# Performance work log

Hardware: AMD Instinct MI355X
Metric: run time of the kernel (lower is better)

## Reference

```python
import jax, jax.numpy as jnp
import numpy as np

N_NODES = 50000
N_EDGES = 800000
IN_F = 64
OUT_F = 64
N_REL = 32
N_BASES = 30


def setup_inputs() -> dict:
    key = jax.random.key(0)
    ks = jax.random.split(key, 6)
    x = jax.random.normal(ks[0], (N_NODES, IN_F), dtype=jnp.float32)
    edge_index = jax.random.randint(ks[1], (2, N_EDGES), 0, N_NODES, dtype=jnp.int64)
    edge_type = jax.random.randint(ks[2], (N_EDGES,), 0, N_REL, dtype=jnp.int64)
    basis = jax.random.normal(ks[3], (N_BASES, IN_F, OUT_F), dtype=jnp.float32) * 0.01
    coeff = jax.random.normal(ks[4], (N_REL, N_BASES), dtype=jnp.float32) * 0.01
    self_weight = jax.random.normal(ks[5], (IN_F, OUT_F), dtype=jnp.float32) * 0.01
    bias = jnp.zeros((OUT_F,), dtype=jnp.float32)
    return {"x": x, "edge_index": edge_index, "edge_type": edge_type,
            "num_nodes": N_NODES, "basis": basis, "coeff": coeff,
            "self_weight": self_weight, "bias": bias}


def reference(x, edge_index, edge_type, num_nodes, basis, coeff, self_weight, bias):
    # W_r = sum_b coeff[r,b] * basis[b]  -> (R, in, out)
    rel_weight = jnp.einsum('rb,bio->rio', coeff, basis)
    source_idx = edge_index[0]
    target_idx = edge_index[1]
    src_feats = x[source_idx]  # (E, in)

    def body(out, rw_r):
        rw, r = rw_r
        mask = (edge_type == r).astype(jnp.float32)  # (E,)
        msg = (src_feats @ rw) * mask[:, None]       # (E, out)
        return out.at[target_idx].add(msg), None

    out0 = jnp.zeros((num_nodes, rel_weight.shape[-1]), dtype=jnp.float32)
    out, _ = jax.lax.scan(body, out0, (rel_weight, jnp.arange(rel_weight.shape[0])))

    in_degree = jnp.zeros((num_nodes,), dtype=jnp.float32).at[target_idx].add(1.0)
    in_degree = jnp.maximum(in_degree, 1.0)
    out = out / in_degree[:, None]
    out = out + x @ self_weight + bias
    return out
```

## Files before the change

### kernel.cpp

```cpp
#include <hip/hip_runtime.h>
#include <hip/hip_bf16.h>

#define IN_F   64
#define OUT_F  64
#define N_RELS 32
#define N_BAS  30
#define KROW   2048
#define B1CHUNK 4096

typedef __attribute__((ext_vector_type(8))) short short8v;
typedef __attribute__((ext_vector_type(4))) _Float16 half4v;
typedef __attribute__((ext_vector_type(4))) float f32x4;
typedef __attribute__((ext_vector_type(4))) unsigned u32x4;
typedef __attribute__((ext_vector_type(2))) unsigned u32x2;

#define MFMA16(a, b, c) __builtin_amdgcn_mfma_f32_16x16x16f16(a, b, c, 0, 0, 0)

__device__ __forceinline__ int dmin(int a, int b) { return a < b ? a : b; }
__device__ __forceinline__ unsigned short f2bf(float f) {
    __hip_bfloat16 h = __float2bfloat16(f);
    return *(unsigned short*)&h;
}

__global__ void __launch_bounds__(256)
k_prep(const float* __restrict__ basis, const float* __restrict__ sw,
       const float* __restrict__ bias, __hip_bfloat16* __restrict__ bbT,
       const float* __restrict__ x, unsigned* __restrict__ xh,
       const int* __restrict__ tgt, int* __restrict__ gsum,
       int N, int E, int nxp) {
    int bb = blockIdx.x;
    int tid = threadIdx.x;
    if (bb < 512) {
        int idx = bb * 256 + tid;
        int e = idx & 7, lane = (idx >> 3) & 63, s = (idx >> 9) & 15, kq = (idx >> 13) & 3, cb = idx >> 15;
        int l15 = lane & 15, lk = lane >> 4;
        int o = cb * 16 + l15;
        int k = kq * 512 + s * 32 + lk * 8 + e;
        int b = k >> 6, i = k & 63;
        float v;
        if (b < N_BAS)      v = basis[((size_t)b * IN_F + i) * OUT_F + o];
        else if (b == 30)   v = sw[(size_t)i * OUT_F + o];
        else                v = (i == 0) ? bias[o] : 0.f;
        bbT[idx] = __float2bfloat16(v);
    } else if (bb < 512 + nxp) {
        int idx = (bb - 512) * 256 + tid;
        if (idx < (N + 1) * 32) {
            int g = idx & 31, n = idx >> 5;
            unsigned v = 0;
            if (n < N) {
                int f = (g & 15) + ((g >> 4) << 5);
                _Float16 lo = (_Float16)x[((size_t)n << 6) + f];
                _Float16 hi = (_Float16)x[((size_t)n << 6) + f + 16];
                v = (unsigned)*(unsigned short*)&lo | ((unsigned)*(unsigned short*)&hi << 16);
            }
            xh[idx] = v;
        }
    } else {
        __shared__ int lh[256];
        int vb = bb - 512 - nxp;
        lh[tid] = 0;
        __syncthreads();
        for (int i = vb * 256 + tid; i < E; i += 256 * 256)
            atomicAdd(&lh[tgt[i] >> 8], 1);
        __syncthreads();
        if (lh[tid]) atomicAdd(&gsum[tid], lh[tid]);
    }
}

__global__ void k_scanB(const int* __restrict__ gsum, int* __restrict__ gexcl,
                        int* __restrict__ bcur, int* __restrict__ off, int NB, int N) {
    int l = threadIdx.x;
    int a0 = (4*l+0 < NB) ? gsum[4*l+0] : 0;
    int a1 = (4*l+1 < NB) ? gsum[4*l+1] : 0;
    int a2 = (4*l+2 < NB) ? gsum[4*l+2] : 0;
    int a3 = (4*l+3 < NB) ? gsum[4*l+3] : 0;
    int s = a0 + a1 + a2 + a3;
    int sc = s;
    for (int d = 1; d < 64; d <<= 1) {
        int o = __shfl_up(sc, d, 64);
        if (l >= d) sc += o;
    }
    int base = sc - s;
    if (4*l+0 < NB) { gexcl[4*l+0] = base;          bcur[4*l+0] = base; }
    if (4*l+1 < NB) { gexcl[4*l+1] = base+a0;       bcur[4*l+1] = base+a0; }
    if (4*l+2 < NB) { gexcl[4*l+2] = base+a0+a1;    bcur[4*l+2] = base+a0+a1; }
    if (4*l+3 < NB) { gexcl[4*l+3] = base+a0+a1+a2; bcur[4*l+3] = base+a0+a1+a2; }
    if (l == 63) { gexcl[NB] = sc; off[N] = sc; }
}

__global__ void __launch_bounds__(1024)
k_b1(const int* __restrict__ src, const int* __restrict__ tgt, const int* __restrict__ et,
     int* __restrict__ bcur, unsigned* __restrict__ ssr, int E) {
    __shared__ unsigned ls_p[B1CHUNK];
    __shared__ unsigned char ls_b[B1CHUNK];
    __shared__ int lh[256], lbase[256], gbase[256], lcur[256];
    int tid = threadIdx.x;
    int e0 = blockIdx.x * B1CHUNK;
    int n = E - e0; if (n > B1CHUNK) n = B1CHUNK;
    if (tid < 256) { lh[tid] = 0; lcur[tid] = 0; }
    __syncthreads();
    unsigned pr[4]; int br[4];
#pragma unroll
    for (int k = 0; k < 4; ++k) {
        int i = k * 1024 + tid;
        br[k] = -1;
        if (i < n) {
            int t = tgt[e0 + i];
            br[k] = t >> 8;
            pr[k] = ((unsigned)(t & 255) << 21) | ((unsigned)src[e0 + i] << 5) | (unsigned)et[e0 + i];
            atomicAdd(&lh[br[k]], 1);
        }
    }
    __syncthreads();
    if (tid < 64) {
        int a0 = lh[4*tid], a1 = lh[4*tid+1], a2 = lh[4*tid+2], a3 = lh[4*tid+3];
        int s = a0 + a1 + a2 + a3, sc = s;
        for (int d = 1; d < 64; d <<= 1) {
            int o = __shfl_up(sc, d, 64);
            if (tid >= d) sc += o;
        }
        int base = sc - s;
        lbase[4*tid] = base; lbase[4*tid+1] = base+a0;
        lbase[4*tid+2] = base+a0+a1; lbase[4*tid+3] = base+a0+a1+a2;
    }
    __syncthreads();
    if (tid < 256 && lh[tid]) gbase[tid] = atomicAdd(&bcur[tid], lh[tid]);
    __syncthreads();
#pragma unroll
    for (int k = 0; k < 4; ++k) {
        if (br[k] >= 0) {
            int pos = atomicAdd(&lcur[br[k]], 1);
            int s = lbase[br[k]] + pos;
            ls_p[s] = pr[k];
            ls_b[s] = (unsigned char)br[k];
        }
    }
    __syncthreads();
#pragma unroll
    for (int k = 0; k < 4; ++k) {
        int i = k * 1024 + tid;
        if (i < n) {
            int b = ls_b[i];
            ssr[gbase[b] + (i - lbase[b])] = ls_p[i];
        }
    }
}

__global__ void __launch_bounds__(256)
k_b2(const unsigned* __restrict__ ssr, const int* __restrict__ gexcl,
     int* __restrict__ off, unsigned* __restrict__ ssr2, int N) {
    __shared__ int lh[256], lofs[256], lcur[256];
    int g = blockIdx.x, tid = threadIdx.x;
    int o0 = gexcl[g], o1 = gexcl[g + 1];
    lh[tid] = 0;
    __syncthreads();
    for (int i = o0 + tid; i < o1; i += 256)
        atomicAdd(&lh[ssr[i] >> 21], 1);
    __syncthreads();
    if (tid < 64) {
        int a0 = lh[4*tid], a1 = lh[4*tid+1], a2 = lh[4*tid+2], a3 = lh[4*tid+3];
        int s = a0 + a1 + a2 + a3, sc = s;
        for (int d = 1; d < 64; d <<= 1) {
            int o = __shfl_up(sc, d, 64);
            if (tid >= d) sc += o;
        }
        int base = sc - s;
        lofs[4*tid] = base; lofs[4*tid+1] = base+a0;
        lofs[4*tid+2] = base+a0+a1; lofs[4*tid+3] = base+a0+a1+a2;
    }
    __syncthreads();
    int t = (g << 8) + tid;
    if (t < N) off[t] = o0 + lofs[tid];
    lcur[tid] = o0 + lofs[tid];
    __syncthreads();
    for (int i = o0 + tid; i < o1; i += 256) {
        unsigned p = ssr[i];
        int pos = atomicAdd(&lcur[p >> 21], 1);
        ssr2[pos] = p;
    }
}

__device__ __forceinline__ void edge_round(
    unsigned char* zb, const unsigned* cofs2, const unsigned* est,
    const unsigned* __restrict__ ssr2, const char* __restrict__ xhB,
    int tIdx, int s0r, int s1r, float xselfv,
    int mh, int l15, int lk, unsigned xadd2, unsigned cbase, u32x4 w0)
{
    int deg = s1r - s0r;
    int sbase = lk << 2;
    f32x4 acc00 = {0.f,0.f,0.f,0.f};
    f32x4 acc01 = acc00, acc10 = acc00, acc11 = acc00;
    if (deg > 0) {
        if (deg <= 128) {
            int nt = (deg + 15) >> 4;
#pragma unroll 1
            for (int kt = 0; kt < nt; ++kt) {
                u32x4 wn = w0;
                if (kt + 1 < nt)
                    wn = *(const u32x4*)((const unsigned char*)(est + tIdx * 128 + (kt + 1) * 16 + sbase));
                union { unsigned short u[4]; half4v h; } bf0, bf1, a0, a1;
#pragma unroll
                for (int j = 0; j < 4; ++j) {
                    unsigned wj = w0[j];
                    unsigned bw = cofs2[cbase + ((wj & 31u) << 4) + l15];
                    unsigned xw = *(const unsigned*)(xhB + (((size_t)((wj >> 5) & 0xFFFFu)) << 7) + xadd2);
                    bf0.u[j] = (unsigned short)(bw & 0xFFFFu);
                    bf1.u[j] = (unsigned short)(bw >> 16);
                    a0.u[j]  = (unsigned short)(xw & 0xFFFFu);
                    a1.u[j]  = (unsigned short)(xw >> 16);
                }
                acc00 = MFMA16(a0.h, bf0.h, acc00);
                acc01 = MFMA16(a0.h, bf1.h, acc01);
                acc10 = MFMA16(a1.h, bf0.h, acc10);
                acc11 = MFMA16(a1.h, bf1.h, acc11);
                w0 = wn;
            }
        } else {
            int last = s1r - 1;
#pragma unroll 1
            for (int kt = 0; kt * 16 < deg; ++kt) {
                int rem = deg - kt * 16;
                unsigned ew = ssr2[dmin(s0r + kt * 16 + l15, last)];
                union { unsigned short u[4]; half4v h; } bf0, bf1, a0, a1;
#pragma unroll
                for (int j = 0; j < 4; ++j) {
                    unsigned wj = (unsigned)__builtin_amdgcn_ds_bpermute((lk << 4) + j * 4, (int)ew);
                    bool okj = (sbase + j) < rem;
                    unsigned rrow = okj ? (wj & 31u) : 32u;
                    unsigned wjs  = okj ? wj : 0u;
                    unsigned bw = cofs2[cbase + (rrow << 4) + l15];
                    unsigned xw = *(const unsigned*)(xhB + (((size_t)((wjs >> 5) & 0xFFFFu)) << 7) + xadd2);
                    bf0.u[j] = (unsigned short)(bw & 0xFFFFu);
                    bf1.u[j] = (unsigned short)(bw >> 16);
                    a0.u[j]  = (unsigned short)(xw & 0xFFFFu);
                    a1.u[j]  = (unsigned short)(xw >> 16);
                }
                acc00 = MFMA16(a0.h, bf0.h, acc00);
                acc01 = MFMA16(a0.h, bf1.h, acc01);
                acc10 = MFMA16(a1.h, bf0.h, acc10);
                acc11 = MFMA16(a1.h, bf1.h, acc11);
            }
        }
    }
    float inv = 1.f / fmaxf((float)deg, 1.f);
    unsigned rb = (unsigned)tIdx << 12;
    unsigned swz = (unsigned)((tIdx & 7) << 4);
    unsigned ib = (unsigned)((mh << 5) + (lk << 2));
    {
        unsigned short h0, h1, h2, h3;
        u32x2 pv;
        h0 = f2bf(acc00[0]*inv); h1 = f2bf(acc00[1]*inv); h2 = f2bf(acc00[2]*inv); h3 = f2bf(acc00[3]*inv);
        pv[0] = h0 | ((unsigned)h1 << 16); pv[1] = h2 | ((unsigned)h3 << 16);
        unsigned byt = ((unsigned)l15 << 7) + (ib << 1);
        byt ^= swz ^ (((byt >> 7) & 7) << 4);
        *(u32x2*)(zb + rb + byt) = pv;
        h0 = f2bf(acc01[0]*inv); h1 = f2bf(acc01[1]*inv); h2 = f2bf(acc01[2]*inv); h3 = f2bf(acc01[3]*inv);
        pv[0] = h0 | ((unsigned)h1 << 16); pv[1] = h2 | ((unsigned)h3 << 16);
        byt = ((unsigned)(16 + l15) << 7) + (ib << 1);
        byt ^= swz ^ (((byt >> 7) & 7) << 4);
        *(u32x2*)(zb + rb + byt) = pv;
        h0 = f2bf(acc10[0]*inv); h1 = f2bf(acc10[1]*inv); h2 = f2bf(acc10[2]*inv); h3 = f2bf(acc10[3]*inv);
        pv[0] = h0 | ((unsigned)h1 << 16); pv[1] = h2 | ((unsigned)h3 << 16);
        byt = ((unsigned)l15 << 7) + ((ib + 16) << 1);
        byt ^= swz ^ (((byt >> 7) & 7) << 4);
        *(u32x2*)(zb + rb + byt) = pv;
        h0 = f2bf(acc11[0]*inv); h1 = f2bf(acc11[1]*inv); h2 = f2bf(acc11[2]*inv); h3 = f2bf(acc11[3]*inv);
        pv[0] = h0 | ((unsigned)h1 << 16); pv[1] = h2 | ((unsigned)h3 << 16);
        byt = ((unsigned)(16 + l15) << 7) + ((ib + 16) << 1);
        byt ^= swz ^ (((byt >> 7) & 7) << 4);
        *(u32x2*)(zb + rb + byt) = pv;
    }
    int lane = (lk << 4) + l15;
    if (lane < 32) {
        unsigned byt = (30u << 7) + ((unsigned)((mh << 5) + lane) << 1);
        byt ^= swz ^ (((byt >> 7) & 7) << 4);
        *(unsigned short*)(zb + rb + byt) = f2bf(xselfv);
        if (mh == 0 && lane == 0) {
            unsigned byb = (31u << 7);
            byb ^= swz ^ (((byb >> 7) & 7) << 4);
            *(unsigned short*)(zb + rb + byb) = (unsigned short)0x3F80;
        }
    }
}

__global__ void __launch_bounds__(1024, 8)
k_fused(const float* __restrict__ x, const unsigned* __restrict__ xh,
        const unsigned* __restrict__ ssr2, const int* __restrict__ off,
        const float* __restrict__ coeff, const __hip_bfloat16* __restrict__ bbT,
        float* __restrict__ out, int N) {
    __shared__ __align__(16) unsigned char zb[16 * 4096];
    __shared__ __align__(16) float pf[16 * 256];
    unsigned* cofs2 = (unsigned*)pf;
    unsigned* est   = ((unsigned*)pf) + 1120;
    int tid = threadIdx.x;
    int w = tid >> 6, lane = tid & 63;
    int mh = w & 1;
    int t0 = blockIdx.x * 16;

    int tA = t0 + (w >> 1), tB = tA + 8;
    int okA = (tA < N), okB = (tB < N);
    int offA0 = okA ? off[tA] : 0;
    int offA1 = okA ? off[tA + 1] : 0;
    int offB0 = okB ? off[tB] : 0;
    int offB1 = okB ? off[tB + 1] : 0;
    float xsA = okA ? x[((size_t)tA << 6) + (mh << 5) + (lane & 31)] : 0.f;
    float xsB = okB ? x[((size_t)tB << 6) + (mh << 5) + (lane & 31)] : 0.f;

    int s0A = __builtin_amdgcn_readfirstlane(offA0);
    int s1A = __builtin_amdgcn_readfirstlane(offA1);
    int s0B = __builtin_amdgcn_readfirstlane(offB0);
    int s1B = __builtin_amdgcn_readfirstlane(offB1);

    for (int idx = tid; idx < 33 * 16; idx += 1024) {
        int r = idx >> 4, c = idx & 15;
        float lo = (r < 32) ? coeff[r * N_BAS + c] : 0.f;
        float hi = (r < 32 && (c + 16) < N_BAS) ? coeff[r * N_BAS + c + 16] : 0.f;
        _Float16 hl = (_Float16)lo, hh = (_Float16)hi;
        unsigned v = (unsigned)*(unsigned short*)&hl | ((unsigned)*(unsigned short*)&hh << 16);
        cofs2[idx] = v;
        cofs2[idx + 560] = v;
    }
    {
        unsigned PADW = (unsigned)N << 5;
        int sgt = mh ? s0B : s0A;
        int sg1 = mh ? s1B : s1A;
        int slot = (w >> 1) + (mh << 3);
        int degS = sg1 - sgt;
        if (degS > 0 && degS <= 128) {
            int pe = (degS + 15) & ~15;
            if (lane < degS)           est[slot * 128 + lane] = ssr2[sgt + lane];
            else if (lane < pe)        est[slot * 128 + lane] = PADW;
            if (lane + 64 < degS)      est[slot * 128 + lane + 64] = ssr2[sgt + lane + 64];
            else if (lane + 64 < pe)   est[slot * 128 + lane + 64] = PADW;
        }
    }
    __syncthreads();

    int l15 = lane & 15, lk = lane >> 4;
    int sbase = lk << 2;
    unsigned xadd2 = (unsigned)(((mh << 4) + l15) << 2);
    const char* xhB = (const char*)xh;
    unsigned cbase = (unsigned)((lk & 1) * 560);

    int degA = s1A - s0A, degB = s1B - s0B;
    u32x4 wA0 = {0u, 0u, 0u, 0u}, wB0 = {0u, 0u, 0u, 0u};
    if (degA > 0 && degA <= 128)
        wA0 = *(const u32x4*)((const unsigned char*)(est + (w >> 1) * 128 + sbase));
    if (degB > 0 && degB <= 128)
        wB0 = *(const u32x4*)((const unsigned char*)(est + ((w >> 1) + 8) * 128 + sbase));

    edge_round(zb, cofs2, est, ssr2, xhB, (w >> 1),     s0A, s1A, xsA,
               mh, l15, lk, xadd2, cbase, wA0);
    edge_round(zb, cofs2, est, ssr2, xhB, (w >> 1) + 8, s0B, s1B, xsB,
               mh, l15, lk, xadd2, cbase, wB0);
    __syncthreads();

    {
        int colblk = w & 3, kq = w >> 2;
        const char* bp2 = (const char*)bbT + (((unsigned)(colblk * 4 + kq)) << 14) + ((unsigned)lane << 4);
        unsigned arow = (unsigned)l15 << 12;
        unsigned aswz = (unsigned)((l15 & 7) << 4);
        f32x4 acc2 = {0.f,0.f,0.f,0.f};
#pragma unroll 4
        for (int s = 0; s < 16; ++s) {
            unsigned abyte = (unsigned)((kq << 10) + (s << 6) + (lk << 4));
            abyte ^= aswz ^ (((abyte >> 7) & 7) << 4);
            short8v a = *(const short8v*)(zb + arow + abyte);
            short8v b = *(const short8v*)(bp2 + (s << 10));
            acc2 = __builtin_amdgcn_mfma_f32_16x16x32_bf16(a, b, acc2, 0, 0, 0);
        }
#pragma unroll
        for (int q = 0; q < 4; ++q)
            pf[(w << 8) + ((lk << 2) + q) * 16 + l15] = acc2[q];
    }
    __syncthreads();

    {
        int row = w, col = lane;
        int cb = col >> 4, cl = col & 15;
        int tt = t0 + row;
        if (tt < N) {
            float v = pf[(((0 << 2) + cb) << 8) + (row << 4) + cl]
                    + pf[(((1 << 2) + cb) << 8) + (row << 4) + cl]
                    + pf[(((2 << 2) + cb) << 8) + (row << 4) + cl]
                    + pf[(((3 << 2) + cb) << 8) + (row << 4) + cl];
            out[((size_t)tt << 6) + col] = v;
        }
    }
}

extern "C" void kernel_launch(void* const* d_in, const int* in_sizes, int n_in,
                              void* d_out, int out_size, void* d_ws, size_t ws_size,
                              hipStream_t stream) {
    const float* x     = (const float*)d_in[0];
    const int*   eidx  = (const int*)d_in[1];
    const int*   etype = (const int*)d_in[2];
    const float* basis = (const float*)d_in[4];
    const float* coeff = (const float*)d_in[5];
    const float* sw    = (const float*)d_in[6];
    const float* bias  = (const float*)d_in[7];

    const int E = in_sizes[1] / 2;
    const int N = out_size / OUT_F;
    const int NB = (N + 255) >> 8;
    const int* srcv = eidx;
    const int* tgtv = eidx + E;
    float* out = (float*)d_out;

    size_t p = 0;
    auto alloc = [&](size_t bytes) { size_t cur = p; p += (bytes + 255) & ~(size_t)255; return cur; };
    char* base = (char*)d_ws;
    __hip_bfloat16* bbT   = (__hip_bfloat16*)(base + alloc((size_t)OUT_F * KROW * 2));
    int*            gsum  = (int*)(base + alloc(256 * 4));
    int*            gexcl = (int*)(base + alloc((size_t)(NB + 1) * 4));
    int*            bcur  = (int*)(base + alloc((size_t)NB * 4));
    int*            off   = (int*)(base + alloc((size_t)(N + 1) * 4));
    unsigned*       ssr   = (unsigned*)(base + alloc((size_t)E * 4));
    unsigned*       ssr2  = (unsigned*)(base + alloc((size_t)E * 4));
    unsigned*       xh    = (unsigned*)(base + alloc((size_t)(N + 1) * 32 * 4));
    (void)ws_size;

    hipMemsetAsync(gsum, 0, 256 * 4, stream);

    const int nxp = ((N + 1) * 32 + 255) >> 8;
    k_prep<<<512 + nxp + 256, 256, 0, stream>>>(basis, sw, bias, bbT, x, xh, tgtv, gsum, N, E, nxp);
    k_scanB<<<1, 64, 0, stream>>>(gsum, gexcl, bcur, off, NB, N);
    k_b1<<<(E + B1CHUNK - 1) / B1CHUNK, 1024, 0, stream>>>(srcv, tgtv, etype, bcur, ssr, E);
    k_b2<<<NB, 256, 0, stream>>>(ssr, gexcl, off, ssr2, N);
    k_fused<<<(N + 15) / 16, 1024, 0, stream>>>(x, xh, ssr2, off, coeff, bbT, out, N);
}
```

Before: 109.7 us.

## Replace two-pass bucket sort with per-node atomic counting sort for CSR build

Builds the target-sorted edge list by counting in-degree per node with global atomics, computing per-node offsets via block sums and scans, and scattering each edge directly with a global atomic cursor. This removes the intermediate bucketed buffer and the second LDS-based sort pass. In exchange it relies on many scattered global atomics and adds two small kernels, and the edge order within a node becomes nondeterministic.

```diff
diff --git a/kernel.cpp b/kernel.cpp
--- a/kernel.cpp
+++ b/kernel.cpp
@@ -6,7 +6,6 @@
 #define N_RELS 32
 #define N_BAS  30
 #define KROW   2048
-#define B1CHUNK 4096
 
 typedef __attribute__((ext_vector_type(8))) short short8v;
 typedef __attribute__((ext_vector_type(4))) _Float16 half4v;
@@ -26,7 +25,7 @@
 k_prep(const float* __restrict__ basis, const float* __restrict__ sw,
        const float* __restrict__ bias, __hip_bfloat16* __restrict__ bbT,
        const float* __restrict__ x, unsigned* __restrict__ xh,
-       const int* __restrict__ tgt, int* __restrict__ gsum,
+       const int* __restrict__ tgt, int* __restrict__ cnt,
        int N, int E, int nxp) {
     int bb = blockIdx.x;
     int tid = threadIdx.x;
@@ -56,19 +55,28 @@
             xh[idx] = v;
         }
     } else {
-        __shared__ int lh[256];
         int vb = bb - 512 - nxp;
-        lh[tid] = 0;
+        for (int i = vb * 256 + tid; i < E; i += 256 * 256)
+            atomicAdd(&cnt[tgt[i]], 1);
+    }
+}
+
+__global__ void __launch_bounds__(256)
+k_sum256(const int* __restrict__ cnt, int* __restrict__ gsum, int N) {
+    __shared__ int lh[256];
+    int b = blockIdx.x, tid = threadIdx.x;
+    int t = (b << 8) + tid;
+    lh[tid] = (t < N) ? cnt[t] : 0;
+    __syncthreads();
+    for (int s = 128; s > 0; s >>= 1) {
+        if (tid < s) lh[tid] += lh[tid + s];
         __syncthreads();
-        for (int i = vb * 256 + tid; i < E; i += 256 * 256)
-            atomicAdd(&lh[tgt[i] >> 8], 1);
-        __syncthreads();
-        if (lh[tid]) atomicAdd(&gsum[tid], lh[tid]);
-    }
+    }
+    if (tid == 0) gsum[b] = lh[0];
 }
 
 __global__ void k_scanB(const int* __restrict__ gsum, int* __restrict__ gexcl,
-                        int* __restrict__ bcur, int* __restrict__ off, int NB, int N) {
+                        int* __restrict__ off, int NB, int N) {
     int l = threadIdx.x;
     int a0 = (4*l+0 < NB) ? gsum[4*l+0] : 0;
     int a1 = (4*l+1 < NB) ? gsum[4*l+1] : 0;
@@ -81,36 +89,20 @@
         if (l >= d) sc += o;
     }
     int base = sc - s;
-    if (4*l+0 < NB) { gexcl[4*l+0] = base;          bcur[4*l+0] = base; }
-    if (4*l+1 < NB) { gexcl[4*l+1] = base+a0;       bcur[4*l+1] = base+a0; }
-    if (4*l+2 < NB) { gexcl[4*l+2] = base+a0+a1;    bcur[4*l+2] = base+a0+a1; }
-    if (4*l+3 < NB) { gexcl[4*l+3] = base+a0+a1+a2; bcur[4*l+3] = base+a0+a1+a2; }
+    if (4*l+0 < NB) gexcl[4*l+0] = base;
+    if (4*l+1 < NB) gexcl[4*l+1] = base+a0;
+    if (4*l+2 < NB) gexcl[4*l+2] = base+a0+a1;
+    if (4*l+3 < NB) gexcl[4*l+3] = base+a0+a1+a2;
     if (l == 63) { gexcl[NB] = sc; off[N] = sc; }
 }
 
-__global__ void __launch_bounds__(1024)
-k_b1(const int* __restrict__ src, const int* __restrict__ tgt, const int* __restrict__ et,
-     int* __restrict__ bcur, unsigned* __restrict__ ssr, int E) {
-    __shared__ unsigned ls_p[B1CHUNK];
-    __shared__ unsigned char ls_b[B1CHUNK];
-    __shared__ int lh[256], lbase[256], gbase[256], lcur[256];
-    int tid = threadIdx.x;
-    int e0 = blockIdx.x * B1CHUNK;
-    int n = E - e0; if (n > B1CHUNK) n = B1CHUNK;
-    if (tid < 256) { lh[tid] = 0; lcur[tid] = 0; }
-    __syncthreads();
-    unsigned pr[4]; int br[4];
-#pragma unroll
-    for (int k = 0; k < 4; ++k) {
-        int i = k * 1024 + tid;
-        br[k] = -1;
-        if (i < n) {
-            int t = tgt[e0 + i];
-            br[k] = t >> 8;
-            pr[k] = ((unsigned)(t & 255) << 21) | ((unsigned)src[e0 + i] << 5) | (unsigned)et[e0 + i];
-            atomicAdd(&lh[br[k]], 1);
-        }
-    }
+__global__ void __launch_bounds__(256)
+k_off(const int* __restrict__ cnt, const int* __restrict__ gexcl,
+      int* __restrict__ off, int* __restrict__ tcur, int N) {
+    __shared__ int lh[256], lofs[256];
+    int b = blockIdx.x, tid = threadIdx.x;
+    int t = (b << 8) + tid;
+    lh[tid] = (t < N) ? cnt[t] : 0;
     __syncthreads();
     if (tid < 64) {
         int a0 = lh[4*tid], a1 = lh[4*tid+1], a2 = lh[4*tid+2], a3 = lh[4*tid+3];
@@ -120,63 +112,25 @@
             if (tid >= d) sc += o;
         }
         int base = sc - s;
-        lbase[4*tid] = base; lbase[4*tid+1] = base+a0;
-        lbase[4*tid+2] = base+a0+a1; lbase[4*tid+3] = base+a0+a1+a2;
-    }
-    __syncthreads();
-    if (tid < 256 && lh[tid]) gbase[tid] = atomicAdd(&bcur[tid], lh[tid]);
-    __syncthreads();
-#pragma unroll
-    for (int k = 0; k < 4; ++k) {
-        if (br[k] >= 0) {
-            int pos = atomicAdd(&lcur[br[k]], 1);
-            int s = lbase[br[k]] + pos;
-            ls_p[s] = pr[k];
-            ls_b[s] = (unsigned char)br[k];
-        }
-    }
-    __syncthreads();
-#pragma unroll
-    for (int k = 0; k < 4; ++k) {
-        int i = k * 1024 + tid;
-        if (i < n) {
-            int b = ls_b[i];
-            ssr[gbase[b] + (i - lbase[b])] = ls_p[i];
-        }
-    }
-}
-
-__global__ void __launch_bounds__(256)
-k_b2(const unsigned* __restrict__ ssr, const int* __restrict__ gexcl,
-     int* __restrict__ off, unsigned* __restrict__ ssr2, int N) {
-    __shared__ int lh[256], lofs[256], lcur[256];
-    int g = blockIdx.x, tid = threadIdx.x;
-    int o0 = gexcl[g], o1 = gexcl[g + 1];
-    lh[tid] = 0;
-    __syncthreads();
-    for (int i = o0 + tid; i < o1; i += 256)
-        atomicAdd(&lh[ssr[i] >> 21], 1);
-    __syncthreads();
-    if (tid < 64) {
-        int a0 = lh[4*tid], a1 = lh[4*tid+1], a2 = lh[4*tid+2], a3 = lh[4*tid+3];
-        int s = a0 + a1 + a2 + a3, sc = s;
-        for (int d = 1; d < 64; d <<= 1) {
-            int o = __shfl_up(sc, d, 64);
-            if (tid >= d) sc += o;
-        }
-        int base = sc - s;
         lofs[4*tid] = base; lofs[4*tid+1] = base+a0;
         lofs[4*tid+2] = base+a0+a1; lofs[4*tid+3] = base+a0+a1+a2;
     }
     __syncthreads();
-    int t = (g << 8) + tid;
-    if (t < N) off[t] = o0 + lofs[tid];
-    lcur[tid] = o0 + lofs[tid];
-    __syncthreads();
-    for (int i = o0 + tid; i < o1; i += 256) {
-        unsigned p = ssr[i];
-        int pos = atomicAdd(&lcur[p >> 21], 1);
-        ssr2[pos] = p;
+    if (t < N) {
+        int v = gexcl[b] + lofs[tid];
+        off[t] = v;
+        tcur[t] = v;
+    }
+}
+
+__global__ void __launch_bounds__(256)
+k_scatter(const int* __restrict__ src, const int* __restrict__ tgt, const int* __restrict__ et,
+          int* __restrict__ tcur, unsigned* __restrict__ ssr2, int E) {
+    int i = blockIdx.x * 256 + threadIdx.x;
+    if (i < E) {
+        int t = tgt[i];
+        int pos = atomicAdd(&tcur[t], 1);
+        ssr2[pos] = ((unsigned)src[i] << 5) | (unsigned)et[i];
     }
 }
 
@@ -412,20 +366,21 @@
     char* base = (char*)d_ws;
     __hip_bfloat16* bbT   = (__hip_bfloat16*)(base + alloc((size_t)OUT_F * KROW * 2));
     int*            gsum  = (int*)(base + alloc(256 * 4));
+    int*            cnt   = (int*)(base + alloc((size_t)N * 4));
     int*            gexcl = (int*)(base + alloc((size_t)(NB + 1) * 4));
-    int*            bcur  = (int*)(base + alloc((size_t)NB * 4));
     int*            off   = (int*)(base + alloc((size_t)(N + 1) * 4));
-    unsigned*       ssr   = (unsigned*)(base + alloc((size_t)E * 4));
+    int*            tcur  = (int*)(base + alloc((size_t)N * 4));
     unsigned*       ssr2  = (unsigned*)(base + alloc((size_t)E * 4));
     unsigned*       xh    = (unsigned*)(base + alloc((size_t)(N + 1) * 32 * 4));
     (void)ws_size;
 
-    hipMemsetAsync(gsum, 0, 256 * 4, stream);
+    hipMemsetAsync(gsum, 0, 1024 + (size_t)N * 4, stream);
 
     const int nxp = ((N + 1) * 32 + 255) >> 8;
-    k_prep<<<512 + nxp + 256, 256, 0, stream>>>(basis, sw, bias, bbT, x, xh, tgtv, gsum, N, E, nxp);
-    k_scanB<<<1, 64, 0, stream>>>(gsum, gexcl, bcur, off, NB, N);
-    k_b1<<<(E + B1CHUNK - 1) / B1CHUNK, 1024, 0, stream>>>(srcv, tgtv, etype, bcur, ssr, E);
-    k_b2<<<NB, 256, 0, stream>>>(ssr, gexcl, off, ssr2, N);
+    k_prep<<<512 + nxp + 256, 256, 0, stream>>>(basis, sw, bias, bbT, x, xh, tgtv, cnt, N, E, nxp);
+    k_sum256<<<NB, 256, 0, stream>>>(cnt, gsum, N);
+    k_scanB<<<1, 64, 0, stream>>>(gsum, gexcl, off, NB, N);
+    k_off<<<NB, 256, 0, stream>>>(cnt, gexcl, off, tcur, N);
+    k_scatter<<<(E + 255) / 256, 256, 0, stream>>>(srcv, tgtv, etype, tcur, ssr2, E);
     k_fused<<<(N + 15) / 16, 1024, 0, stream>>>(x, xh, ssr2, off, coeff, bbT, out, N);
 }
```

Result: slower. 175.3 us (+59.9%).

## Software-prefetch x gathers one tile ahead and widen bucket-sort blocks

Applied to the files above, without the earlier changes.

The edge loop in the fused kernel now issues the global gathers of source features for the next 16-edge tile before running the MFMAs of the current tile. The first tile of the second target group is gathered before the first group is processed, so those loads overlap earlier work. Separately, the second bucket-sort kernel runs with 1024 threads per block instead of 256 to get more parallelism per bucket. The prefetch adds register pressure, and the larger blocks contend more on shared-memory atomics.

```diff
diff --git a/kernel.cpp b/kernel.cpp
--- a/kernel.cpp
+++ b/kernel.cpp
@@ -146,15 +146,15 @@
     }
 }
 
-__global__ void __launch_bounds__(256)
+__global__ void __launch_bounds__(1024)
 k_b2(const unsigned* __restrict__ ssr, const int* __restrict__ gexcl,
      int* __restrict__ off, unsigned* __restrict__ ssr2, int N) {
     __shared__ int lh[256], lofs[256], lcur[256];
     int g = blockIdx.x, tid = threadIdx.x;
     int o0 = gexcl[g], o1 = gexcl[g + 1];
-    lh[tid] = 0;
-    __syncthreads();
-    for (int i = o0 + tid; i < o1; i += 256)
+    if (tid < 256) lh[tid] = 0;
+    __syncthreads();
+    for (int i = o0 + tid; i < o1; i += 1024)
         atomicAdd(&lh[ssr[i] >> 21], 1);
     __syncthreads();
     if (tid < 64) {
@@ -169,22 +169,52 @@
         lofs[4*tid+2] = base+a0+a1; lofs[4*tid+3] = base+a0+a1+a2;
     }
     __syncthreads();
-    int t = (g << 8) + tid;
-    if (t < N) off[t] = o0 + lofs[tid];
-    lcur[tid] = o0 + lofs[tid];
-    __syncthreads();
-    for (int i = o0 + tid; i < o1; i += 256) {
+    if (tid < 256) {
+        int t = (g << 8) + tid;
+        if (t < N) off[t] = o0 + lofs[tid];
+        lcur[tid] = o0 + lofs[tid];
+    }
+    __syncthreads();
+    for (int i = o0 + tid; i < o1; i += 1024) {
         unsigned p = ssr[i];
         int pos = atomicAdd(&lcur[p >> 21], 1);
         ssr2[pos] = p;
     }
 }
 
+__device__ __forceinline__ u32x4 gather4(const char* __restrict__ xhB, unsigned xadd2, u32x4 wv) {
+    u32x4 xv;
+#pragma unroll
+    for (int j = 0; j < 4; ++j)
+        xv[j] = *(const unsigned*)(xhB + (((size_t)((wv[j] >> 5) & 0xFFFFu)) << 7) + xadd2);
+    return xv;
+}
+
+__device__ __forceinline__ void tile_mfma(
+    const unsigned* cofs2, unsigned cbase, int l15, u32x4 wv, u32x4 xv,
+    f32x4& acc00, f32x4& acc01, f32x4& acc10, f32x4& acc11)
+{
+    union { unsigned short u[4]; half4v h; } bf0, bf1, a0, a1;
+#pragma unroll
+    for (int j = 0; j < 4; ++j) {
+        unsigned bw = cofs2[cbase + ((wv[j] & 31u) << 4) + l15];
+        bf0.u[j] = (unsigned short)(bw & 0xFFFFu);
+        bf1.u[j] = (unsigned short)(bw >> 16);
+        a0.u[j]  = (unsigned short)(xv[j] & 0xFFFFu);
+        a1.u[j]  = (unsigned short)(xv[j] >> 16);
+    }
+    acc00 = MFMA16(a0.h, bf0.h, acc00);
+    acc01 = MFMA16(a0.h, bf1.h, acc01);
+    acc10 = MFMA16(a1.h, bf0.h, acc10);
+    acc11 = MFMA16(a1.h, bf1.h, acc11);
+}
+
+template<bool PF>
 __device__ __forceinline__ void edge_round(
     unsigned char* zb, const unsigned* cofs2, const unsigned* est,
     const unsigned* __restrict__ ssr2, const char* __restrict__ xhB,
     int tIdx, int s0r, int s1r, float xselfv,
-    int mh, int l15, int lk, unsigned xadd2, unsigned cbase, u32x4 w0)
+    int mh, int l15, int lk, unsigned xadd2, unsigned cbase, u32x4 w0, u32x4 xw0)
 {
     int deg = s1r - s0r;
     int sbase = lk << 2;
@@ -193,27 +223,16 @@
     if (deg > 0) {
         if (deg <= 128) {
             int nt = (deg + 15) >> 4;
+            u32x4 xv0 = PF ? xw0 : gather4(xhB, xadd2, w0);
 #pragma unroll 1
             for (int kt = 0; kt < nt; ++kt) {
-                u32x4 wn = w0;
-                if (kt + 1 < nt)
+                u32x4 wn = w0, xn = xv0;
+                if (kt + 1 < nt) {
                     wn = *(const u32x4*)((const unsigned char*)(est + tIdx * 128 + (kt + 1) * 16 + sbase));
-                union { unsigned short u[4]; half4v h; } bf0, bf1, a0, a1;
-#pragma unroll
-                for (int j = 0; j < 4; ++j) {
-                    unsigned wj = w0[j];
-                    unsigned bw = cofs2[cbase + ((wj & 31u) << 4) + l15];
-                    unsigned xw = *(const unsigned*)(xhB + (((size_t)((wj >> 5) & 0xFFFFu)) << 7) + xadd2);
-                    bf0.u[j] = (unsigned short)(bw & 0xFFFFu);
-                    bf1.u[j] = (unsigned short)(bw >> 16);
-                    a0.u[j]  = (unsigned short)(xw & 0xFFFFu);
-                    a1.u[j]  = (unsigned short)(xw >> 16);
+                    xn = gather4(xhB, xadd2, wn);
                 }
-                acc00 = MFMA16(a0.h, bf0.h, acc00);
-                acc01 = MFMA16(a0.h, bf1.h, acc01);
-                acc10 = MFMA16(a1.h, bf0.h, acc10);
-                acc11 = MFMA16(a1.h, bf1.h, acc11);
-                w0 = wn;
+                tile_mfma(cofs2, cbase, l15, w0, xv0, acc00, acc01, acc10, acc11);
+                w0 = wn; xv0 = xn;
             }
         } else {
             int last = s1r - 1;
@@ -344,15 +363,18 @@
 
     int degA = s1A - s0A, degB = s1B - s0B;
     u32x4 wA0 = {0u, 0u, 0u, 0u}, wB0 = {0u, 0u, 0u, 0u};
+    u32x4 xB0 = {0u, 0u, 0u, 0u};
     if (degA > 0 && degA <= 128)
         wA0 = *(const u32x4*)((const unsigned char*)(est + (w >> 1) * 128 + sbase));
-    if (degB > 0 && degB <= 128)
+    if (degB > 0 && degB <= 128) {
         wB0 = *(const u32x4*)((const unsigned char*)(est + ((w >> 1) + 8) * 128 + sbase));
-
-    edge_round(zb, cofs2, est, ssr2, xhB, (w >> 1),     s0A, s1A, xsA,
-               mh, l15, lk, xadd2, cbase, wA0);
-    edge_round(zb, cofs2, est, ssr2, xhB, (w >> 1) + 8, s0B, s1B, xsB,
-               mh, l15, lk, xadd2, cbase, wB0);
+        xB0 = gather4(xhB, xadd2, wB0);
+    }
+
+    edge_round<false>(zb, cofs2, est, ssr2, xhB, (w >> 1),     s0A, s1A, xsA,
+                      mh, l15, lk, xadd2, cbase, wA0, xB0 );
+    edge_round<true>(zb, cofs2, est, ssr2, xhB, (w >> 1) + 8, s0B, s1B, xsB,
+                     mh, l15, lk, xadd2, cbase, wB0, xB0);
     __syncthreads();
 
     {
@@ -426,6 +448,6 @@
     k_prep<<<512 + nxp + 256, 256, 0, stream>>>(basis, sw, bias, bbT, x, xh, tgtv, gsum, N, E, nxp);
     k_scanB<<<1, 64, 0, stream>>>(gsum, gexcl, bcur, off, NB, N);
     k_b1<<<(E + B1CHUNK - 1) / B1CHUNK, 1024, 0, stream>>>(srcv, tgtv, etype, bcur, ssr, E);
-    k_b2<<<NB, 256, 0, stream>>>(ssr, gexcl, off, ssr2, N);
+    k_b2<<<NB, 1024, 0, stream>>>(ssr, gexcl, off, ssr2, N);
     k_fused<<<(N + 15) / 16, 1024, 0, stream>>>(x, xh, ssr2, off, coeff, bbT, out, N);
 }
```

Measured after the change: 106.7 us. 1.03x faster.
